# Performance work log

Hardware: AMD Instinct MI355X
Metric: run time of the kernel (lower is better)

## Reference

```python
import jax, jax.numpy as jnp
import numpy as np

N_E = 1024
E_DIM = 256
BETA = 0.25

def setup_inputs() -> dict:
    key = jax.random.key(0)
    k1, k2 = jax.random.split(key)
    z = jax.random.normal(k1, (32, E_DIM, 32, 32), dtype=jnp.float32)
    # embedding initialized uniform(-1/n_e, 1/n_e) as in the torch module
    emb_w = jax.random.uniform(k2, (N_E, E_DIM), dtype=jnp.float32,
                               minval=-1.0 / N_E, maxval=1.0 / N_E)
    return {"z": z, "emb_w": emb_w}

def reference(z, emb_w):
    # z: (B, C, H, W) with C == e_dim
    zp = jnp.transpose(z, (0, 2, 3, 1))          # (B, H, W, C)
    zf = zp.reshape(-1, emb_w.shape[1])           # (N, e_dim)
    # squared L2 distances: ||z||^2 + ||e||^2 - 2 z e^T  -> (N, n_e)
    d = (jnp.sum(zf * zf, axis=1, keepdims=True)
         + jnp.sum(emb_w * emb_w, axis=1)
         - 2.0 * jnp.matmul(zf, emb_w.T))
    idx = jnp.argmin(d, axis=1)                   # (N,)
    min_encoding_indices = idx[:, None]           # (N, 1)
    min_encodings = jax.nn.one_hot(idx, emb_w.shape[0], dtype=zf.dtype)  # (N, n_e)
    z_q = emb_w[idx].reshape(zp.shape)            # gather instead of one-hot matmul
    # VQ loss (stop-gradient on codebook / encoder respectively)
    loss = (jnp.mean((jax.lax.stop_gradient(z_q) - zp) ** 2)
            + BETA * jnp.mean((z_q - jax.lax.stop_gradient(zp)) ** 2))
    # straight-through estimator
    z_q_st = zp + jax.lax.stop_gradient(z_q - zp)
    e_mean = jnp.mean(min_encodings, axis=0)      # (n_e,)
    perplexity = jnp.exp(-jnp.sum(e_mean * jnp.log(e_mean + 1e-10)))
    z_q_out = jnp.transpose(z_q_st, (0, 3, 1, 2)) # (B, C, H, W)
    return (z_q_out, loss, perplexity, min_encodings, min_encoding_indices)
```

## Files before the change

kernel.cpp:

```cpp
#include <hip/hip_runtime.h>
#include <math.h>

#define NROWS 32768
#define NE    1024
#define CDIM  256
#define ZB_STRIDE 262144

#define ZQ_OFF   0
#define LOSS_OFF 8388608
#define PERP_OFF 8388609
#define ENC_OFF  8388610
#define IDX_OFF  41943042

#define THETA 1.0e-4f
#define NEG2_SCALE (-0.00048828125f)

typedef _Float16 f16x8 __attribute__((ext_vector_type(8)));
typedef __attribute__((ext_vector_type(4))) float f32x4;
typedef __attribute__((ext_vector_type(8))) unsigned short ushort8;

__device__ __forceinline__ unsigned short f2h(float x) {
  _Float16 h = (_Float16)x;
  unsigned short u;
  __builtin_memcpy(&u, &h, 2);
  return u;
}

__device__ __forceinline__ float np_sumsq_256_s1(const float* __restrict__ base) {
  float tot[2];
#pragma unroll
  for (int hh = 0; hh < 2; ++hh) {
    float r[8];
#pragma unroll
    for (int j = 0; j < 8; ++j) {
      float x = base[hh * 128 + j];
      r[j] = __fmul_rn(x, x);
    }
    for (int i = 8; i < 128; i += 8) {
#pragma unroll
      for (int j = 0; j < 8; ++j) {
        float x = base[hh * 128 + i + j];
        r[j] = __fadd_rn(r[j], __fmul_rn(x, x));
      }
    }
    tot[hh] = __fadd_rn(__fadd_rn(__fadd_rn(r[0], r[1]), __fadd_rn(r[2], r[3])),
                        __fadd_rn(__fadd_rn(r[4], r[5]), __fadd_rn(r[6], r[7])));
  }
  return __fadd_rn(tot[0], tot[1]);
}

__global__ __launch_bounds__(256) void convert_all(const float* __restrict__ z,
                                                   const float* __restrict__ emb,
                                                   unsigned short* __restrict__ zf16r,
                                                   unsigned short* __restrict__ ef16r,
                                                   float* __restrict__ embT,
                                                   float* __restrict__ znorm,
                                                   float* __restrict__ enorm) {
  __shared__ __align__(16) char smem[38144];
  const int bid = blockIdx.x;
  const int t = threadIdx.x;

  if (bid < 512) {
    unsigned short (*T16)[266] = reinterpret_cast<unsigned short (*)[266]>(smem);
    float (*accsF)[8][16][4] = reinterpret_cast<float (*)[8][16][4]>(smem + 34048);
    const int b = bid >> 4, hwt = bid & 15;
    const int hw0 = hwt * 64;
    const int hw4 = t & 15;
    const int jj = (t >> 4) & 7;
    const int hh = t >> 7;
    const float* zb = z + (size_t)b * ZB_STRIDE + hw0 + hw4 * 4;

    float rr[4];
#pragma unroll
    for (int i = 0; i < 16; ++i) {
      int c = hh * 128 + jj + 8 * i;
      float4 v = *reinterpret_cast<const float4*>(zb + (size_t)c * 1024);
      const float xv[4] = {v.x, v.y, v.z, v.w};
#pragma unroll
      for (int q = 0; q < 4; ++q) {
        float p = __fmul_rn(xv[q], xv[q]);
        rr[q] = (i == 0) ? p : __fadd_rn(rr[q], p);
        T16[hw4 * 4 + q][c] = f2h(xv[q]);
      }
    }
#pragma unroll
    for (int q = 0; q < 4; ++q) accsF[hh][jj][hw4][q] = rr[q];
    __syncthreads();

    if (t < 64) {
      const int h4 = t >> 2, cq = t & 3;
      float tot[2];
#pragma unroll
      for (int half = 0; half < 2; ++half) {
        float r[8];
#pragma unroll
        for (int j = 0; j < 8; ++j) r[j] = accsF[half][j][h4][cq];
        tot[half] = __fadd_rn(__fadd_rn(__fadd_rn(r[0], r[1]), __fadd_rn(r[2], r[3])),
                              __fadd_rn(__fadd_rn(r[4], r[5]), __fadd_rn(r[6], r[7])));
      }
      znorm[b * 1024 + hw0 + t] = __fadd_rn(tot[0], tot[1]);
    }

    const int pw = b * 16 + hwt;
    const int panel = pw >> 1, wrh = pw & 1;
    const int l15w = t & 15, gw = (t >> 4) & 3, miw = t >> 6;
    const int rowW = miw * 16 + l15w;
#pragma unroll
    for (int kc = 0; kc < 8; ++kc) {
      ushort8 o;
#pragma unroll
      for (int el = 0; el < 8; ++el) o[el] = T16[rowW][kc * 32 + gw * 8 + el];
      size_t chunk = ((((size_t)panel * 2 + wrh) * 8 + kc) * 4 + miw) * 64 + (size_t)gw * 16 + l15w;
      *reinterpret_cast<ushort8*>(zf16r + (chunk << 3)) = o;
    }
  } else if (bid < 640) {
    int cid = (bid - 512) * 256 + t;
    int e = cid >> 5, cc = cid & 31;
    int kc = cc >> 2, g = cc & 3;
    int c0 = kc * 32 + g * 8;
    ushort8 o;
#pragma unroll
    for (int el = 0; el < 8; ++el) o[el] = f2h(emb[(size_t)e * 256 + c0 + el] * 4096.0f);
    int et = e >> 7, wcb = (e >> 6) & 1, nj = (e >> 4) & 3, l15e = e & 15;
    size_t chunk = ((((size_t)et * 2 + wcb) * 8 + kc) * 4 + nj) * 64 + (size_t)g * 16 + l15e;
    *reinterpret_cast<ushort8*>(ef16r + (chunk << 3)) = o;
  } else if (bid < 896) {
    float (*tile)[33] = reinterpret_cast<float (*)[33]>(smem);
    int tb = bid - 640;
    int be = tb & 31, bc = tb >> 5;
    int tx = t & 31, ty = t >> 5;
#pragma unroll
    for (int i = 0; i < 4; ++i)
      tile[ty + 8 * i][tx] = emb[(size_t)(be * 32 + ty + 8 * i) * 256 + bc * 32 + tx];
    __syncthreads();
#pragma unroll
    for (int i = 0; i < 4; ++i)
      embT[(size_t)(bc * 32 + ty + 8 * i) * 1024 + be * 32 + tx] = tile[tx][ty + 8 * i];
  } else {
    int n = (bid - 896) * 256 + t;
    enorm[n] = np_sumsq_256_s1(emb + (size_t)n * CDIM);
  }
}

__global__ __launch_bounds__(256, 4) void argmin_tile(
    const unsigned short* __restrict__ zf16r, const unsigned short* __restrict__ ef16r,
    const float* __restrict__ znorm, const float* __restrict__ enorm,
    int* __restrict__ idx_out, float* __restrict__ loss_blk,
    int* __restrict__ flag_cnt, int* __restrict__ flag_list) {
  __shared__ float sdd[64][4];
  __shared__ float sd2[64][4];
  __shared__ int   sdi[64][4];

  const int tid = threadIdx.x;
  const int lane = tid & 63, w = tid >> 6;
  const int l15 = lane & 15, g = lane >> 4;

  const int bid = blockIdx.x;
  const int mb = (bid & 7) * 64 + (bid >> 3);
  const int n0 = mb * 64;

  const unsigned short* bP0 = zf16r + (size_t)mb * 16384 + lane * 8;

  float zn[4];
#pragma unroll
  for (int nj = 0; nj < 4; ++nj) zn[nj] = znorm[n0 + nj * 16 + l15];

  float bd[4], b2[4]; int bi[4];
#pragma unroll
  for (int nj = 0; nj < 4; ++nj) { bd[nj] = 3.4e38f; b2[nj] = 3.4e38f; bi[nj] = 0; }

  const f32x4 z4 = {0.f, 0.f, 0.f, 0.f};
#pragma unroll 1
  for (int et = 0; et < 4; ++et) {
    const unsigned short* aP = ef16r + (size_t)(w * 4 + et) * 16384 + lane * 8;
    const unsigned short* bP = bP0;

    f32x4 acc[4][4];
#pragma unroll
    for (int ei = 0; ei < 4; ++ei)
#pragma unroll
      for (int nj = 0; nj < 4; ++nj) acc[ei][nj] = z4;

#pragma unroll 1
    for (int kc = 0; kc < 8; ++kc) {
      f16x8 af[4], bv[4];
#pragma unroll
      for (int ei = 0; ei < 4; ++ei)
        af[ei] = *reinterpret_cast<const f16x8*>(aP + ei * 512);
#pragma unroll
      for (int nj = 0; nj < 4; ++nj)
        bv[nj] = *reinterpret_cast<const f16x8*>(bP + nj * 512);
      aP += 2048; bP += 2048;
#pragma unroll
      for (int ei = 0; ei < 4; ++ei)
#pragma unroll
        for (int nj = 0; nj < 4; ++nj)
          acc[ei][nj] = __builtin_amdgcn_mfma_f32_16x16x32_f16(af[ei], bv[nj],
                                                               acc[ei][nj], 0, 0, 0);
    }

    const int e0w = (w * 4 + et) * 64;
#pragma unroll
    for (int ei = 0; ei < 4; ++ei)
#pragma unroll
      for (int rg = 0; rg < 4; ++rg) {
        int e = e0w + ei * 16 + g * 4 + rg;
        float en = enorm[e];
#pragma unroll
        for (int nj = 0; nj < 4; ++nj) {
          float d = fmaf(NEG2_SCALE, acc[ei][nj][rg], __fadd_rn(zn[nj], en));
          if (d < bd[nj]) {
            b2[nj] = bd[nj]; bd[nj] = d; bi[nj] = e;
          } else if (d < b2[nj]) {
            b2[nj] = d;
          }
        }
      }
  }

#pragma unroll
  for (int nj = 0; nj < 4; ++nj) {
#pragma unroll
    for (int m = 16; m <= 32; m <<= 1) {
      float od = __shfl_xor(bd[nj], m, 64);
      int   oi = __shfl_xor(bi[nj], m, 64);
      float o2 = __shfl_xor(b2[nj], m, 64);
      float hi = fmaxf(bd[nj], od);
      b2[nj] = fminf(fminf(b2[nj], o2), hi);
      if (od < bd[nj] || (od == bd[nj] && oi < bi[nj])) { bd[nj] = od; bi[nj] = oi; }
    }
    if (g == 0) {
      int nl = nj * 16 + l15;
      sdd[nl][w] = bd[nj];
      sdi[nl][w] = bi[nj];
      sd2[nl][w] = b2[nj];
    }
  }
  __syncthreads();

  if (tid < 64) {
    float bdf = 3.4e38f; int bif = 0x7FFFFFFF; int bw = -1;
#pragma unroll
    for (int ww = 0; ww < 4; ++ww) {
      float d = sdd[tid][ww];
      int   i = sdi[tid][ww];
      if (d < bdf || (d == bdf && i < bif)) { bdf = d; bif = i; bw = ww; }
    }
    float b2f = 3.4e38f;
#pragma unroll
    for (int ww = 0; ww < 4; ++ww) {
      float v = (ww == bw) ? sd2[tid][ww] : sdd[tid][ww];
      b2f = fminf(b2f, v);
    }
    int n = n0 + tid;
    idx_out[n] = bif;
    if (b2f - bdf < THETA) {
      int p = atomicAdd(flag_cnt, 1);
      flag_list[p] = n;
    }
    float s = bdf;
#pragma unroll
    for (int m = 1; m <= 32; m <<= 1) s += __shfl_xor(s, m, 64);
    if (tid == 0) loss_blk[bid] = s;
  }
}

__global__ __launch_bounds__(256) void repair_kernel(
    const float* __restrict__ z, const float* __restrict__ embT,
    const float* __restrict__ znorm, const float* __restrict__ enorm,
    const int* __restrict__ flag_cnt, const int* __restrict__ flag_list,
    int* __restrict__ idx_out) {
  __shared__ float zrow[4][256];
  __shared__ float rd[256];
  __shared__ int   ri[256];
  const int t = threadIdx.x;
  const int cnt = flag_cnt[0] < NROWS ? flag_cnt[0] : NROWS;
  const int nquad = (cnt + 3) >> 2;
  const float4* embT4 = reinterpret_cast<const float4*>(embT);
  for (int j = blockIdx.x; j < nquad; j += gridDim.x) {
    int nr[4];
    __syncthreads();
#pragma unroll
    for (int r = 0; r < 4; ++r) {
      int jr = j * 4 + r;
      nr[r] = flag_list[jr < cnt ? jr : cnt - 1];
      zrow[r][t] = z[(size_t)(nr[r] >> 10) * ZB_STRIDE + (size_t)t * 1024 + (nr[r] & 1023)];
    }
    __syncthreads();
    float4 dot[4] = {{0.f,0.f,0.f,0.f},{0.f,0.f,0.f,0.f},{0.f,0.f,0.f,0.f},{0.f,0.f,0.f,0.f}};
    for (int k = 0; k < 256; ++k) {
      float4 v = embT4[k * 256 + t];
#pragma unroll
      for (int r = 0; r < 4; ++r) {
        float s = zrow[r][k];
        dot[r].x = fmaf(s, v.x, dot[r].x);
        dot[r].y = fmaf(s, v.y, dot[r].y);
        dot[r].z = fmaf(s, v.z, dot[r].z);
        dot[r].w = fmaf(s, v.w, dot[r].w);
      }
    }
#pragma unroll 1
    for (int r = 0; r < 4; ++r) {
      const float zn = znorm[nr[r]];
      float bd = 3.4e38f; int bi = 0;
      const float dv[4] = {dot[r].x, dot[r].y, dot[r].z, dot[r].w};
#pragma unroll
      for (int q = 0; q < 4; ++q) {
        int e = t * 4 + q;
        float d = __fsub_rn(__fadd_rn(zn, enorm[e]), __fmul_rn(2.0f, dv[q]));
        if (d < bd) { bd = d; bi = e; }
      }
      rd[t] = bd; ri[t] = bi;
      __syncthreads();
      for (int s2 = 128; s2 > 0; s2 >>= 1) {
        if (t < s2) {
          float od = rd[t + s2]; int oi = ri[t + s2];
          if (od < rd[t] || (od == rd[t] && oi < ri[t])) { rd[t] = od; ri[t] = oi; }
        }
        __syncthreads();
      }
      if (t == 0) idx_out[nr[r]] = ri[0];
      __syncthreads();
    }
  }
}

__global__ __launch_bounds__(256) void outputs_kernel(const int* __restrict__ idx,
                                                      const float* __restrict__ emb,
                                                      float* __restrict__ out_enc,
                                                      float* __restrict__ out_idxf,
                                                      int* __restrict__ hist,
                                                      float* __restrict__ zq_out) {
  const int t = threadIdx.x;
  for (int i = blockIdx.x * 256 + t; i < NROWS * 256; i += 2048 * 256) {
    int n = i >> 8, j4 = i & 255;
    int e = idx[n];
    float4 v = {0.f, 0.f, 0.f, 0.f};
    if ((e >> 2) == j4) ((float*)&v)[e & 3] = 1.0f;
    reinterpret_cast<float4*>(out_enc)[i] = v;
  }
  if (blockIdx.x < 1024) {
    __shared__ int   sidx[32];
    __shared__ float erow[32][257];
    int b = blockIdx.x >> 5, h = blockIdx.x & 31;
    if (t < 32) sidx[t] = idx[b * 1024 + h * 32 + t];
    __syncthreads();
    const float4* emb4 = reinterpret_cast<const float4*>(emb);
    int rj = t >> 3, v0 = t & 7;
    int er = sidx[rj];
#pragma unroll
    for (int u = 0; u < 8; ++u) {
      int f4 = v0 + 8 * u;
      float4 vv = emb4[(size_t)er * 64 + f4];
      erow[rj][f4 * 4 + 0] = vv.x;
      erow[rj][f4 * 4 + 1] = vv.y;
      erow[rj][f4 * 4 + 2] = vv.z;
      erow[rj][f4 * 4 + 3] = vv.w;
    }
    __syncthreads();
    int w4 = t & 7, cs = t >> 3;
    float4* zq4 = reinterpret_cast<float4*>(zq_out + (size_t)b * ZB_STRIDE + h * 32);
#pragma unroll
    for (int u = 0; u < 8; ++u) {
      int c = cs + 32 * u;
      float4 o = {erow[w4 * 4 + 0][c], erow[w4 * 4 + 1][c],
                  erow[w4 * 4 + 2][c], erow[w4 * 4 + 3][c]};
      zq4[(size_t)c * 256 + w4] = o;
    }
  } else if (blockIdx.x < 1152) {
    int n = (blockIdx.x - 1024) * 256 + t;
    int e = idx[n];
    out_idxf[n] = (float)e;
    atomicAdd(&hist[e], 1);
  }
}

__global__ __launch_bounds__(256) void finalize_kernel(const float* __restrict__ loss_blk,
                                                       const int* __restrict__ hist,
                                                       float* __restrict__ out_loss,
                                                       float* __restrict__ out_perp) {
  __shared__ float red[256];
  int t = threadIdx.x;
  red[t] = loss_blk[t] + loss_blk[t + 256];
  __syncthreads();
  for (int s2 = 128; s2 > 0; s2 >>= 1) {
    if (t < s2) red[t] += red[t + s2];
    __syncthreads();
  }
  if (t == 0) out_loss[0] = 1.25f * (red[0] / 8388608.0f);
  __syncthreads();
  float hs = 0.f;
  for (int i = t; i < 1024; i += 256) {
    float em = (float)hist[i] / 32768.0f;
    hs += em * logf(em + 1e-10f);
  }
  red[t] = hs;
  __syncthreads();
  for (int s2 = 128; s2 > 0; s2 >>= 1) {
    if (t < s2) red[t] += red[t + s2];
    __syncthreads();
  }
  if (t == 0) out_perp[0] = expf(-red[0]);
}

extern "C" void kernel_launch(void* const* d_in, const int* in_sizes, int n_in,
                              void* d_out, int out_size, void* d_ws, size_t ws_size,
                              hipStream_t stream) {
  const float* z   = (const float*)d_in[0];
  const float* emb = (const float*)d_in[1];
  float* out = (float*)d_out;

  float* out_zq   = out + ZQ_OFF;
  float* out_loss = out + LOSS_OFF;
  float* out_perp = out + PERP_OFF;
  float* out_enc  = out + ENC_OFF;
  float* out_idxf = out + IDX_OFF;

  int*   idx       = (int*)d_ws;
  int*   hist      = idx + NROWS;
  int*   flag_cnt  = hist + NE;
  int*   flag_list = flag_cnt + 4;
  float* loss_blk  = (float*)(flag_list + NROWS);
  float* znorm     = loss_blk + 512;
  float* enorm     = znorm + NROWS;

  unsigned short* zf16r = (unsigned short*)(out_enc + 2);
  unsigned short* ef16r = zf16r + (size_t)NROWS * CDIM;
  float*          embT  = (float*)(ef16r + (size_t)NE * CDIM);

  hipMemsetAsync(hist, 0, (NE + 1) * sizeof(int), stream);

  convert_all<<<900, 256, 0, stream>>>(z, emb, zf16r, ef16r, embT, znorm, enorm);
  argmin_tile<<<512, 256, 0, stream>>>(zf16r, ef16r, znorm, enorm,
                                       idx, loss_blk, flag_cnt, flag_list);
  repair_kernel<<<256, 256, 0, stream>>>(z, embT, znorm, enorm, flag_cnt, flag_list, idx);
  outputs_kernel<<<2048, 256, 0, stream>>>(idx, emb, out_enc, out_idxf, hist, out_zq);
  finalize_kernel<<<1, 256, 0, stream>>>(loss_blk, hist, out_loss, out_perp);
}
```

Measured before the change: 153.4 us.

## Fuse z fp16 conversion into argmin kernel with shared-memory B fragments

```diff
diff --git a/kernel.cpp b/kernel.cpp
--- a/kernel.cpp
+++ b/kernel.cpp
@@ -49,27 +49,68 @@
   return __fadd_rn(tot[0], tot[1]);
 }
 
-__global__ __launch_bounds__(256) void convert_all(const float* __restrict__ z,
-                                                   const float* __restrict__ emb,
-                                                   unsigned short* __restrict__ zf16r,
-                                                   unsigned short* __restrict__ ef16r,
-                                                   float* __restrict__ embT,
-                                                   float* __restrict__ znorm,
-                                                   float* __restrict__ enorm) {
-  __shared__ __align__(16) char smem[38144];
+__global__ __launch_bounds__(256) void prep_e(const float* __restrict__ emb,
+                                              unsigned short* __restrict__ ef16r,
+                                              float* __restrict__ embT,
+                                              float* __restrict__ enorm) {
   const int bid = blockIdx.x;
   const int t = threadIdx.x;
-
-  if (bid < 512) {
-    unsigned short (*T16)[266] = reinterpret_cast<unsigned short (*)[266]>(smem);
-    float (*accsF)[8][16][4] = reinterpret_cast<float (*)[8][16][4]>(smem + 34048);
-    const int b = bid >> 4, hwt = bid & 15;
-    const int hw0 = hwt * 64;
+  if (bid < 128) {
+    int cid = bid * 256 + t;
+    int e = cid >> 5, cc = cid & 31;
+    int kc = cc >> 2, g = cc & 3;
+    int c0 = kc * 32 + g * 8;
+    ushort8 o;
+#pragma unroll
+    for (int el = 0; el < 8; ++el) o[el] = f2h(emb[(size_t)e * 256 + c0 + el] * 4096.0f);
+    int et = e >> 7, wcb = (e >> 6) & 1, nj = (e >> 4) & 3, l15e = e & 15;
+    size_t chunk = ((((size_t)et * 2 + wcb) * 8 + kc) * 4 + nj) * 64 + (size_t)g * 16 + l15e;
+    *reinterpret_cast<ushort8*>(ef16r + (chunk << 3)) = o;
+  } else if (bid < 384) {
+    __shared__ float tile[32][33];
+    int tb = bid - 128;
+    int be = tb & 31, bc = tb >> 5;
+    int tx = t & 31, ty = t >> 5;
+#pragma unroll
+    for (int i = 0; i < 4; ++i)
+      tile[ty + 8 * i][tx] = emb[(size_t)(be * 32 + ty + 8 * i) * 256 + bc * 32 + tx];
+    __syncthreads();
+#pragma unroll
+    for (int i = 0; i < 4; ++i)
+      embT[(size_t)(bc * 32 + ty + 8 * i) * 1024 + be * 32 + tx] = tile[tx][ty + 8 * i];
+  } else {
+    int n = (bid - 384) * 256 + t;
+    enorm[n] = np_sumsq_256_s1(emb + (size_t)n * CDIM);
+  }
+}
+
+__global__ __launch_bounds__(512, 4) void zconv_argmin(
+    const float* __restrict__ z, const unsigned short* __restrict__ ef16r,
+    const float* __restrict__ enorm, float* __restrict__ znorm,
+    int* __restrict__ idx_out, float* __restrict__ loss_blk,
+    int* __restrict__ flag_cnt, int* __restrict__ flag_list) {
+  __shared__ __align__(16) char smA[34048];
+  __shared__ float accsF[2][8][16][4];
+  __shared__ float znl[64];
+  __shared__ float sdd[64][8];
+  __shared__ float sd2[64][8];
+  __shared__ int   sdi[64][8];
+
+  const int t = threadIdx.x;
+  const int bid = blockIdx.x;
+  const int mb = (bid & 7) * 64 + (bid >> 3);
+  const int n0 = mb * 64;
+  const int b = mb >> 4, hwt = mb & 15;
+  const int hw0 = hwt * 64;
+
+  unsigned short (*T16)[266] = reinterpret_cast<unsigned short (*)[266]>(smA);
+  unsigned short* Bfrag = reinterpret_cast<unsigned short*>(smA);
+
+  if (t < 256) {
     const int hw4 = t & 15;
     const int jj = (t >> 4) & 7;
     const int hh = t >> 7;
     const float* zb = z + (size_t)b * ZB_STRIDE + hw0 + hw4 * 4;
-
     float rr[4];
 #pragma unroll
     for (int i = 0; i < 16; ++i) {
@@ -85,85 +126,53 @@
     }
 #pragma unroll
     for (int q = 0; q < 4; ++q) accsF[hh][jj][hw4][q] = rr[q];
-    __syncthreads();
-
-    if (t < 64) {
-      const int h4 = t >> 2, cq = t & 3;
-      float tot[2];
-#pragma unroll
-      for (int half = 0; half < 2; ++half) {
-        float r[8];
-#pragma unroll
-        for (int j = 0; j < 8; ++j) r[j] = accsF[half][j][h4][cq];
-        tot[half] = __fadd_rn(__fadd_rn(__fadd_rn(r[0], r[1]), __fadd_rn(r[2], r[3])),
-                              __fadd_rn(__fadd_rn(r[4], r[5]), __fadd_rn(r[6], r[7])));
-      }
-      znorm[b * 1024 + hw0 + t] = __fadd_rn(tot[0], tot[1]);
-    }
-
-    const int pw = b * 16 + hwt;
-    const int panel = pw >> 1, wrh = pw & 1;
-    const int l15w = t & 15, gw = (t >> 4) & 3, miw = t >> 6;
+  }
+  __syncthreads();
+
+  if (t < 64) {
+    const int h4 = t >> 2, cq = t & 3;
+    float tot[2];
+#pragma unroll
+    for (int half = 0; half < 2; ++half) {
+      float r[8];
+#pragma unroll
+      for (int j = 0; j < 8; ++j) r[j] = accsF[half][j][h4][cq];
+      tot[half] = __fadd_rn(__fadd_rn(__fadd_rn(r[0], r[1]), __fadd_rn(r[2], r[3])),
+                            __fadd_rn(__fadd_rn(r[4], r[5]), __fadd_rn(r[6], r[7])));
+    }
+    float nr = __fadd_rn(tot[0], tot[1]);
+    znl[t] = nr;
+    znorm[n0 + t] = nr;
+  }
+  ushort8 fr[8];
+  {
+    const int l15w = t & 15, gw = (t >> 4) & 3, miw = (t >> 6) & 3;
     const int rowW = miw * 16 + l15w;
+    if (t < 256) {
+#pragma unroll
+      for (int kc = 0; kc < 8; ++kc)
+#pragma unroll
+        for (int el = 0; el < 8; ++el) fr[kc][el] = T16[rowW][kc * 32 + gw * 8 + el];
+    }
+  }
+  __syncthreads();
+
+  if (t < 256) {
+    const int l15w = t & 15, gw = (t >> 4) & 3, miw = (t >> 6) & 3;
 #pragma unroll
     for (int kc = 0; kc < 8; ++kc) {
-      ushort8 o;
-#pragma unroll
-      for (int el = 0; el < 8; ++el) o[el] = T16[rowW][kc * 32 + gw * 8 + el];
-      size_t chunk = ((((size_t)panel * 2 + wrh) * 8 + kc) * 4 + miw) * 64 + (size_t)gw * 16 + l15w;
-      *reinterpret_cast<ushort8*>(zf16r + (chunk << 3)) = o;
-    }
-  } else if (bid < 640) {
-    int cid = (bid - 512) * 256 + t;
-    int e = cid >> 5, cc = cid & 31;
-    int kc = cc >> 2, g = cc & 3;
-    int c0 = kc * 32 + g * 8;
-    ushort8 o;
-#pragma unroll
-    for (int el = 0; el < 8; ++el) o[el] = f2h(emb[(size_t)e * 256 + c0 + el] * 4096.0f);
-    int et = e >> 7, wcb = (e >> 6) & 1, nj = (e >> 4) & 3, l15e = e & 15;
-    size_t chunk = ((((size_t)et * 2 + wcb) * 8 + kc) * 4 + nj) * 64 + (size_t)g * 16 + l15e;
-    *reinterpret_cast<ushort8*>(ef16r + (chunk << 3)) = o;
-  } else if (bid < 896) {
-    float (*tile)[33] = reinterpret_cast<float (*)[33]>(smem);
-    int tb = bid - 640;
-    int be = tb & 31, bc = tb >> 5;
-    int tx = t & 31, ty = t >> 5;
-#pragma unroll
-    for (int i = 0; i < 4; ++i)
-      tile[ty + 8 * i][tx] = emb[(size_t)(be * 32 + ty + 8 * i) * 256 + bc * 32 + tx];
-    __syncthreads();
-#pragma unroll
-    for (int i = 0; i < 4; ++i)
-      embT[(size_t)(bc * 32 + ty + 8 * i) * 1024 + be * 32 + tx] = tile[tx][ty + 8 * i];
-  } else {
-    int n = (bid - 896) * 256 + t;
-    enorm[n] = np_sumsq_256_s1(emb + (size_t)n * CDIM);
-  }
-}
-
-__global__ __launch_bounds__(256, 4) void argmin_tile(
-    const unsigned short* __restrict__ zf16r, const unsigned short* __restrict__ ef16r,
-    const float* __restrict__ znorm, const float* __restrict__ enorm,
-    int* __restrict__ idx_out, float* __restrict__ loss_blk,
-    int* __restrict__ flag_cnt, int* __restrict__ flag_list) {
-  __shared__ float sdd[64][4];
-  __shared__ float sd2[64][4];
-  __shared__ int   sdi[64][4];
-
-  const int tid = threadIdx.x;
-  const int lane = tid & 63, w = tid >> 6;
+      int chunk = (kc * 4 + miw) * 64 + gw * 16 + l15w;
+      *reinterpret_cast<ushort8*>(Bfrag + chunk * 8) = fr[kc];
+    }
+  }
+  __syncthreads();
+
+  const int lane = t & 63, w = t >> 6;
   const int l15 = lane & 15, g = lane >> 4;
 
-  const int bid = blockIdx.x;
-  const int mb = (bid & 7) * 64 + (bid >> 3);
-  const int n0 = mb * 64;
-
-  const unsigned short* bP0 = zf16r + (size_t)mb * 16384 + lane * 8;
-
   float zn[4];
 #pragma unroll
-  for (int nj = 0; nj < 4; ++nj) zn[nj] = znorm[n0 + nj * 16 + l15];
+  for (int nj = 0; nj < 4; ++nj) zn[nj] = znl[nj * 16 + l15];
 
   float bd[4], b2[4]; int bi[4];
 #pragma unroll
@@ -171,9 +180,8 @@
 
   const f32x4 z4 = {0.f, 0.f, 0.f, 0.f};
 #pragma unroll 1
-  for (int et = 0; et < 4; ++et) {
-    const unsigned short* aP = ef16r + (size_t)(w * 4 + et) * 16384 + lane * 8;
-    const unsigned short* bP = bP0;
+  for (int et = 0; et < 2; ++et) {
+    const unsigned short* aP = ef16r + (size_t)(w * 2 + et) * 16384 + lane * 8;
 
     f32x4 acc[4][4];
 #pragma unroll
@@ -189,8 +197,8 @@
         af[ei] = *reinterpret_cast<const f16x8*>(aP + ei * 512);
 #pragma unroll
       for (int nj = 0; nj < 4; ++nj)
-        bv[nj] = *reinterpret_cast<const f16x8*>(bP + nj * 512);
-      aP += 2048; bP += 2048;
+        bv[nj] = *reinterpret_cast<const f16x8*>(Bfrag + ((kc * 4 + nj) * 64 + lane) * 8);
+      aP += 2048;
 #pragma unroll
       for (int ei = 0; ei < 4; ++ei)
 #pragma unroll
@@ -199,7 +207,7 @@
                                                                acc[ei][nj], 0, 0, 0);
     }
 
-    const int e0w = (w * 4 + et) * 64;
+    const int e0w = (w * 2 + et) * 64;
 #pragma unroll
     for (int ei = 0; ei < 4; ++ei)
 #pragma unroll
@@ -238,21 +246,21 @@
   }
   __syncthreads();
 
-  if (tid < 64) {
+  if (t < 64) {
     float bdf = 3.4e38f; int bif = 0x7FFFFFFF; int bw = -1;
 #pragma unroll
-    for (int ww = 0; ww < 4; ++ww) {
-      float d = sdd[tid][ww];
-      int   i = sdi[tid][ww];
+    for (int ww = 0; ww < 8; ++ww) {
+      float d = sdd[t][ww];
+      int   i = sdi[t][ww];
       if (d < bdf || (d == bdf && i < bif)) { bdf = d; bif = i; bw = ww; }
     }
     float b2f = 3.4e38f;
 #pragma unroll
-    for (int ww = 0; ww < 4; ++ww) {
-      float v = (ww == bw) ? sd2[tid][ww] : sdd[tid][ww];
+    for (int ww = 0; ww < 8; ++ww) {
+      float v = (ww == bw) ? sd2[t][ww] : sdd[t][ww];
       b2f = fminf(b2f, v);
     }
-    int n = n0 + tid;
+    int n = n0 + t;
     idx_out[n] = bif;
     if (b2f - bdf < THETA) {
       int p = atomicAdd(flag_cnt, 1);
@@ -261,7 +269,7 @@
     float s = bdf;
 #pragma unroll
     for (int m = 1; m <= 32; m <<= 1) s += __shfl_xor(s, m, 64);
-    if (tid == 0) loss_blk[bid] = s;
+    if (t == 0) loss_blk[bid] = s;
   }
 }
 
@@ -424,15 +432,14 @@
   float* znorm     = loss_blk + 512;
   float* enorm     = znorm + NROWS;
 
-  unsigned short* zf16r = (unsigned short*)(out_enc + 2);
-  unsigned short* ef16r = zf16r + (size_t)NROWS * CDIM;
+  unsigned short* ef16r = (unsigned short*)(out_enc + 2);
   float*          embT  = (float*)(ef16r + (size_t)NE * CDIM);
 
   hipMemsetAsync(hist, 0, (NE + 1) * sizeof(int), stream);
 
-  convert_all<<<900, 256, 0, stream>>>(z, emb, zf16r, ef16r, embT, znorm, enorm);
-  argmin_tile<<<512, 256, 0, stream>>>(zf16r, ef16r, znorm, enorm,
-                                       idx, loss_blk, flag_cnt, flag_list);
+  prep_e<<<388, 256, 0, stream>>>(emb, ef16r, embT, enorm);
+  zconv_argmin<<<512, 512, 0, stream>>>(z, ef16r, enorm, znorm,
+                                        idx, loss_blk, flag_cnt, flag_list);
   repair_kernel<<<256, 256, 0, stream>>>(z, embT, znorm, enorm, flag_cnt, flag_list, idx);
   outputs_kernel<<<2048, 256, 0, stream>>>(idx, emb, out_enc, out_idxf, hist, out_zq);
   finalize_kernel<<<1, 256, 0, stream>>>(loss_blk, hist, out_loss, out_perp);
```

New measurement: 134.8 us. 1.14x faster.
